# Kernel tuning notes

Hardware: AMD Instinct MI355X
Metric: run time of the kernel (lower is better)

## Reference

```python
import jax, jax.numpy as jnp
import numpy as np

NUM_EXPERTS = 8
TOP_K = 2
D_IN = 1024
D_OUT = 1024
N_TOKENS = 8192


def setup_inputs() -> dict:
    key = jax.random.key(0)
    ks = jax.random.split(key, 7)
    s_in = 1.0 / np.sqrt(D_IN)
    s_out = 1.0 / np.sqrt(D_OUT)
    return {
        "x": jax.random.normal(ks[0], (N_TOKENS, D_IN), dtype=jnp.float32),
        # stacked expert params: fc1 [E, D_in, D_out], fc2 [E, D_out, D_out]
        "W1": jax.random.uniform(ks[1], (NUM_EXPERTS, D_IN, D_OUT), jnp.float32, -s_in, s_in),
        "b1": jax.random.uniform(ks[2], (NUM_EXPERTS, D_OUT), jnp.float32, -s_in, s_in),
        "W2": jax.random.uniform(ks[3], (NUM_EXPERTS, D_OUT, D_OUT), jnp.float32, -s_out, s_out),
        "b2": jax.random.uniform(ks[4], (NUM_EXPERTS, D_OUT), jnp.float32, -s_out, s_out),
        "Wg": jax.random.uniform(ks[5], (D_IN, NUM_EXPERTS), jnp.float32, -s_in, s_in),
        "bg": jax.random.uniform(ks[6], (NUM_EXPERTS,), jnp.float32, -s_in, s_in),
    }


def reference(x, W1, b1, W2, b2, Wg, bg):
    n = x.shape[0]
    # gating
    gate_logits = x @ Wg + bg                      # [N, E]
    gate_weights = jax.nn.softmax(gate_logits, axis=1)
    if TOP_K < NUM_EXPERTS:
        topk_vals, topk_idx = jax.lax.top_k(gate_weights, TOP_K)  # [N, K]
        rows = jnp.arange(n)[:, None]
        gate_weights = jnp.zeros_like(gate_weights).at[rows, topk_idx].set(topk_vals)
    # dense all-expert MLP fan-out (faithful to the original wasteful compute)
    h = jax.nn.relu(jnp.einsum('nd,edh->enh', x, W1) + b1[:, None, :])  # [E, N, H]
    y = jnp.einsum('enh,eho->eno', h, W2) + b2[:, None, :]               # [E, N, O]
    # weighted combine over experts
    out = jnp.einsum('ne,eno->no', gate_weights, y)                      # [N, O]
    return out
```

## Files before the change

kernel.cpp:

```cpp
#include <hip/hip_runtime.h>

#define NUM_E 8
#define N_TOK 8192
#define DIM 1024

typedef __attribute__((ext_vector_type(8))) short short8;
typedef __attribute__((ext_vector_type(4))) float f32x4;

__device__ __forceinline__ unsigned short f2bf(float f) {
  unsigned int u = __float_as_uint(f);
  u = (u + 0x7fffu + ((u >> 16) & 1u)) >> 16;
  return (unsigned short)u;
}

__device__ __forceinline__ void async16(const unsigned short* g, unsigned short* l) {
  __builtin_amdgcn_global_load_lds((const __attribute__((address_space(1))) void*)g,
                                   (__attribute__((address_space(3))) void*)l,
                                   16, 0, 0);
}

__global__ __launch_bounds__(256) void convert_w_kernel(const float* __restrict__ W1,
                                                        const float* __restrict__ W2,
                                                        unsigned short* __restrict__ W1T,
                                                        unsigned short* __restrict__ W2T) {
  int tid = blockIdx.x * 256 + threadIdx.x;
  int n   = tid & 1023;
  int kc  = (tid >> 10) & 127;
  int mat = tid >> 17;
  const float* src;
  unsigned short* dst;
  if (mat < 8) { src = W1 + (size_t)mat * (DIM * DIM); dst = W1T + (size_t)mat * (DIM * DIM); }
  else         { src = W2 + (size_t)(mat - 8) * (DIM * DIM); dst = W2T + (size_t)(mat - 8) * (DIM * DIM); }
  const int k0 = kc * 8;
  union { unsigned short u[8]; uint4 v; } o;
#pragma unroll
  for (int j = 0; j < 8; ++j)
    o.u[j] = f2bf(src[(size_t)(k0 + j) * DIM + n]);
  *(uint4*)(dst + (size_t)n * DIM + k0) = o.v;
}

__global__ __launch_bounds__(256) void gate1_kernel(const float* __restrict__ x,
                                                    const float* __restrict__ Wg,
                                                    const float* __restrict__ bg,
                                                    int* __restrict__ tok_top,
                                                    float2* __restrict__ tok_wts,
                                                    unsigned short* __restrict__ xb) {
  const int wave = threadIdx.x >> 6;
  const int lane = threadIdx.x & 63;
  const int n = blockIdx.x * 4 + wave;
  const float4* xr = (const float4*)(x + (size_t)n * DIM);
  unsigned short* xbr = xb + (size_t)n * DIM;
  float acc[NUM_E];
#pragma unroll
  for (int e = 0; e < NUM_E; ++e) acc[e] = 0.f;
#pragma unroll
  for (int it = 0; it < 4; ++it) {
    float4 xv = xr[it * 64 + lane];
    const float4* wr = (const float4*)Wg + (size_t)(it * 256 + lane * 4) * 2;
    float xs[4] = {xv.x, xv.y, xv.z, xv.w};
    union { unsigned short u[4]; uint2 v; } oo;
    oo.u[0] = f2bf(xv.x); oo.u[1] = f2bf(xv.y);
    oo.u[2] = f2bf(xv.z); oo.u[3] = f2bf(xv.w);
    *(uint2*)(xbr + it * 256 + lane * 4) = oo.v;
#pragma unroll
    for (int dd = 0; dd < 4; ++dd) {
      float4 wa = wr[dd * 2 + 0];
      float4 wb = wr[dd * 2 + 1];
      acc[0] += xs[dd] * wa.x; acc[1] += xs[dd] * wa.y;
      acc[2] += xs[dd] * wa.z; acc[3] += xs[dd] * wa.w;
      acc[4] += xs[dd] * wb.x; acc[5] += xs[dd] * wb.y;
      acc[6] += xs[dd] * wb.z; acc[7] += xs[dd] * wb.w;
    }
  }
#pragma unroll
  for (int e = 0; e < NUM_E; ++e)
#pragma unroll
    for (int off = 32; off > 0; off >>= 1)
      acc[e] += __shfl_down(acc[e], off);
  if (lane == 0) {
    float p[NUM_E];
    float mx = -1e30f;
#pragma unroll
    for (int e = 0; e < NUM_E; ++e) { p[e] = acc[e] + bg[e]; mx = fmaxf(mx, p[e]); }
    float s = 0.f;
#pragma unroll
    for (int e = 0; e < NUM_E; ++e) { p[e] = expf(p[e] - mx); s += p[e]; }
    float inv = 1.f / s;
    int i0 = 0;
#pragma unroll
    for (int e = 1; e < NUM_E; ++e) if (p[e] > p[i0]) i0 = e;
    int i1 = (i0 == 0) ? 1 : 0;
#pragma unroll
    for (int e = 0; e < NUM_E; ++e) if (e != i0 && p[e] > p[i1]) i1 = e;
    tok_top[n] = i0 | (i1 << 8);
    tok_wts[n] = make_float2(p[i0] * inv, p[i1] * inv);
  }
}

__global__ __launch_bounds__(1024) void gate2_kernel(const int* __restrict__ tok_top,
                                                     const float2* __restrict__ tok_wts,
                                                     int* __restrict__ counts,
                                                     int* __restrict__ tok_idx,
                                                     float* __restrict__ tok_w) {
  const int e = blockIdx.x;
  const int t = threadIdx.x;
  const int lane = t & 63;
  const int wave = t >> 6;
  __shared__ int wsum[16];
  __shared__ int blocktot;
  int match[8];
  float w[8];
  int cnt = 0;
#pragma unroll
  for (int j = 0; j < 8; ++j) {
    int n = t * 8 + j;
    int top = tok_top[n];
    float2 ww = tok_wts[n];
    bool m0 = (top & 0xff) == e;
    bool m1 = ((top >> 8) & 0xff) == e;
    match[j] = (m0 || m1) ? 1 : 0;
    w[j] = m0 ? ww.x : ww.y;
    cnt += match[j];
  }
  int inc = cnt;
#pragma unroll
  for (int off = 1; off < 64; off <<= 1) {
    int v = __shfl_up(inc, off);
    if (lane >= off) inc += v;
  }
  if (lane == 63) wsum[wave] = inc;
  __syncthreads();
  if (t < 16) {
    int v = wsum[t];
    int s = v;
#pragma unroll
    for (int off = 1; off < 16; off <<= 1) {
      int u = __shfl_up(s, off);
      if (lane >= off) s += u;
    }
    wsum[t] = s - v;
    if (t == 15) blocktot = s;
  }
  __syncthreads();
  int slot = wsum[wave] + inc - cnt;
#pragma unroll
  for (int j = 0; j < 8; ++j) {
    if (match[j]) {
      tok_idx[e * N_TOK + slot] = t * 8 + j;
      tok_w[e * N_TOK + slot] = w[j];
      slot++;
    }
  }
  if (t == 0) counts[e] = blocktot;
}


template <bool FC1>
__global__ __launch_bounds__(256, 3) void moe_gemm_kernel(
    const unsigned short* __restrict__ A_src,
    const unsigned short* __restrict__ wT,
    const float* __restrict__ bias,
    const int* __restrict__ counts,
    const int* __restrict__ tok_idx,
    const float* __restrict__ tok_w,
    unsigned short* __restrict__ h_out,
    float* __restrict__ out)
{
  const int e = blockIdx.x;
  const int count = counts[e];
  const int m0 = blockIdx.z * 128;
  if (m0 >= count) return;
  const int n0 = blockIdx.y * 128;

  int base = 0;
#pragma unroll
  for (int i = 0; i < NUM_E; ++i) base += (i < e) ? ((counts[i] + 127) & ~127) : 0;

  const int tid  = threadIdx.x;
  const int wave = tid >> 6;
  const int lane = tid & 63;
  const int l15  = lane & 15;
  const int quad = lane >> 4;
  const int wm   = wave & 1;
  const int wn   = wave >> 1;

  __shared__ unsigned short sA[3][128 * 32];
  __shared__ unsigned short sB[3][128 * 32];
  __shared__ int   s_tok[128];
  __shared__ float s_w[128];

  if (!FC1) {
    if (tid < 128) {
      int slot = m0 + tid;
      int cs = slot < count ? slot : count - 1;
      s_tok[tid] = tok_idx[e * N_TOK + cs];
      s_w[tid]   = slot < count ? tok_w[e * N_TOK + slot] : 0.f;
    }
    __syncthreads();
  }

  const int r0 = 32 * wave + l15;
  const int r1 = r0 + 16;
  size_t aOff0, aOff1;
  if (FC1) {
    int s0 = m0 + r0; s0 = s0 < count ? s0 : count - 1;
    int s1 = m0 + r1; s1 = s1 < count ? s1 : count - 1;
    aOff0 = (size_t)tok_idx[e * N_TOK + s0] * DIM;
    aOff1 = (size_t)tok_idx[e * N_TOK + s1] * DIM;
  } else {
    aOff0 = (size_t)(base + m0 + r0) * DIM;
    aOff1 = (size_t)(base + m0 + r1) * DIM;
  }
  const unsigned short* wte = wT + (size_t)e * DIM * DIM;
  const size_t bOff0 = (size_t)(n0 + r0) * DIM;
  const size_t bOff1 = (size_t)(n0 + r1) * DIM;
  const int kl = quad * 8;
  const int c0 = (2 * wave + 0) * 512;
  const int c1 = (2 * wave + 1) * 512;

  const f32x4 vzero = {0.f, 0.f, 0.f, 0.f};
  f32x4 acc[4][4];
#pragma unroll
  for (int i = 0; i < 4; ++i)
#pragma unroll
    for (int j = 0; j < 4; ++j) acc[i][j] = vzero;

  auto stage = [&](int kt, int b) {
    const int koff = kt * 32 + kl;
    async16(A_src + aOff0 + koff, &sA[b][c0]);
    async16(A_src + aOff1 + koff, &sA[b][c1]);
    async16(wte + bOff0 + koff, &sB[b][c0]);
    async16(wte + bOff1 + koff, &sB[b][c1]);
  };

  stage(0, 0);
  stage(1, 1);
#pragma unroll
  for (int kt = 0; kt < 32; ++kt) {
    const int cur = kt % 3;
    if (kt + 1 < 32) {
      asm volatile("s_waitcnt vmcnt(4)\n\ts_barrier" ::: "memory");
    } else {
      asm volatile("s_waitcnt vmcnt(0)\n\ts_barrier" ::: "memory");
    }
    if (kt + 2 < 32) stage(kt + 2, (kt + 2) % 3);
    short8 af[4], bfr[4];
#pragma unroll
    for (int i = 0; i < 4; ++i)
      af[i] = *(const short8*)&sA[cur][(wm * 4 + i) * 512 + lane * 8];
#pragma unroll
    for (int j = 0; j < 4; ++j)
      bfr[j] = *(const short8*)&sB[cur][(wn * 4 + j) * 512 + lane * 8];
#pragma unroll
    for (int i = 0; i < 4; ++i)
#pragma unroll
      for (int j = 0; j < 4; ++j)
        acc[i][j] = __builtin_amdgcn_mfma_f32_16x16x32_bf16(af[i], bfr[j], acc[i][j], 0, 0, 0);
  }

  float bv[4];
#pragma unroll
  for (int j = 0; j < 4; ++j)
    bv[j] = bias[e * DIM + n0 + (wn * 4 + j) * 16 + l15];

  if (FC1) {
#pragma unroll
    for (int i = 0; i < 4; ++i) {
      const int rbase = (wm * 4 + i) * 16 + quad * 4;
#pragma unroll
      for (int r = 0; r < 4; ++r) {
        const int slot = m0 + rbase + r;
        if (slot < count) {
          unsigned short* hp = h_out + (size_t)(base + slot) * DIM + n0;
#pragma unroll
          for (int j = 0; j < 4; ++j) {
            float v = acc[i][j][r] + bv[j];
            v = v > 0.f ? v : 0.f;
            hp[(wn * 4 + j) * 16 + l15] = f2bf(v);
          }
        }
      }
    }
  } else {
#pragma unroll
    for (int i = 0; i < 4; ++i) {
      const int rbase = (wm * 4 + i) * 16 + quad * 4;
#pragma unroll
      for (int r = 0; r < 4; ++r) {
        const int slot = m0 + rbase + r;
        if (slot < count) {
          const int rl = rbase + r;
          const int tok = s_tok[rl];
          const float w = s_w[rl];
          float* op = out + (size_t)tok * DIM + n0;
#pragma unroll
          for (int j = 0; j < 4; ++j) {
            float v = acc[i][j][r] + bv[j];
            atomicAdd(&op[(wn * 4 + j) * 16 + l15], w * v);
          }
        }
      }
    }
  }
}


extern "C" void kernel_launch(void* const* d_in, const int* in_sizes, int n_in,
                              void* d_out, int out_size, void* d_ws, size_t ws_size,
                              hipStream_t stream) {
  const float* x  = (const float*)d_in[0];
  const float* W1 = (const float*)d_in[1];
  const float* b1 = (const float*)d_in[2];
  const float* W2 = (const float*)d_in[3];
  const float* b2 = (const float*)d_in[4];
  const float* Wg = (const float*)d_in[5];
  const float* bg = (const float*)d_in[6];
  float* out = (float*)d_out;

  char* ws = (char*)d_ws;
  int*            counts  = (int*)(ws);
  int*            tok_idx = (int*)(ws + 1024);
  float*          tok_w   = (float*)(ws + 263168);
  unsigned short* xb      = (unsigned short*)(ws + 525312);
  unsigned short* w1t     = (unsigned short*)(ws + 525312 + 16777216ull);
  unsigned short* w2t     = (unsigned short*)(ws + 525312 + 2ull * 16777216ull);
  unsigned short* hb      = (unsigned short*)(ws + 525312 + 3ull * 16777216ull);
  size_t gate_off = 525312 + 3ull * 16777216ull + 35651584ull;
  int*            tok_top = (int*)(ws + gate_off);
  float2*         tok_wts = (float2*)(ws + gate_off + 32768);

  hipMemsetAsync(d_out, 0, (size_t)N_TOK * DIM * sizeof(float), stream);

  convert_w_kernel<<<2 * NUM_E * DIM * (DIM / 8) / 256, 256, 0, stream>>>(W1, W2, w1t, w2t);
  gate1_kernel<<<N_TOK / 4, 256, 0, stream>>>(x, Wg, bg, tok_top, tok_wts, xb);
  gate2_kernel<<<NUM_E, 1024, 0, stream>>>(tok_top, tok_wts, counts, tok_idx, tok_w);
  moe_gemm_kernel<true><<<dim3(NUM_E, 8, 64), 256, 0, stream>>>(
      xb, w1t, b1, counts, tok_idx, tok_w, hb, nullptr);
  moe_gemm_kernel<false><<<dim3(NUM_E, 8, 64), 256, 0, stream>>>(
      hb, w2t, b2, counts, tok_idx, tok_w, nullptr, out);
}
```

Baseline: 398.8 us.

## Fuse weight convert and gating into one prep kernel; compact MoE tile grid

```diff
diff --git a/kernel.cpp b/kernel.cpp
--- a/kernel.cpp
+++ b/kernel.cpp
@@ -19,81 +19,91 @@
                                    16, 0, 0);
 }
 
-__global__ __launch_bounds__(256) void convert_w_kernel(const float* __restrict__ W1,
-                                                        const float* __restrict__ W2,
-                                                        unsigned short* __restrict__ W1T,
-                                                        unsigned short* __restrict__ W2T) {
-  int tid = blockIdx.x * 256 + threadIdx.x;
-  int n   = tid & 1023;
-  int kc  = (tid >> 10) & 127;
-  int mat = tid >> 17;
-  const float* src;
-  unsigned short* dst;
-  if (mat < 8) { src = W1 + (size_t)mat * (DIM * DIM); dst = W1T + (size_t)mat * (DIM * DIM); }
-  else         { src = W2 + (size_t)(mat - 8) * (DIM * DIM); dst = W2T + (size_t)(mat - 8) * (DIM * DIM); }
-  const int k0 = kc * 8;
-  union { unsigned short u[8]; uint4 v; } o;
-#pragma unroll
-  for (int j = 0; j < 8; ++j)
-    o.u[j] = f2bf(src[(size_t)(k0 + j) * DIM + n]);
-  *(uint4*)(dst + (size_t)n * DIM + k0) = o.v;
-}
-
-__global__ __launch_bounds__(256) void gate1_kernel(const float* __restrict__ x,
-                                                    const float* __restrict__ Wg,
-                                                    const float* __restrict__ bg,
-                                                    int* __restrict__ tok_top,
-                                                    float2* __restrict__ tok_wts,
-                                                    unsigned short* __restrict__ xb) {
-  const int wave = threadIdx.x >> 6;
-  const int lane = threadIdx.x & 63;
-  const int n = blockIdx.x * 4 + wave;
-  const float4* xr = (const float4*)(x + (size_t)n * DIM);
-  unsigned short* xbr = xb + (size_t)n * DIM;
-  float acc[NUM_E];
-#pragma unroll
-  for (int e = 0; e < NUM_E; ++e) acc[e] = 0.f;
-#pragma unroll
-  for (int it = 0; it < 4; ++it) {
-    float4 xv = xr[it * 64 + lane];
-    const float4* wr = (const float4*)Wg + (size_t)(it * 256 + lane * 4) * 2;
-    float xs[4] = {xv.x, xv.y, xv.z, xv.w};
-    union { unsigned short u[4]; uint2 v; } oo;
-    oo.u[0] = f2bf(xv.x); oo.u[1] = f2bf(xv.y);
-    oo.u[2] = f2bf(xv.z); oo.u[3] = f2bf(xv.w);
-    *(uint2*)(xbr + it * 256 + lane * 4) = oo.v;
-#pragma unroll
-    for (int dd = 0; dd < 4; ++dd) {
-      float4 wa = wr[dd * 2 + 0];
-      float4 wb = wr[dd * 2 + 1];
-      acc[0] += xs[dd] * wa.x; acc[1] += xs[dd] * wa.y;
-      acc[2] += xs[dd] * wa.z; acc[3] += xs[dd] * wa.w;
-      acc[4] += xs[dd] * wb.x; acc[5] += xs[dd] * wb.y;
-      acc[6] += xs[dd] * wb.z; acc[7] += xs[dd] * wb.w;
-    }
-  }
-#pragma unroll
-  for (int e = 0; e < NUM_E; ++e)
-#pragma unroll
-    for (int off = 32; off > 0; off >>= 1)
-      acc[e] += __shfl_down(acc[e], off);
-  if (lane == 0) {
-    float p[NUM_E];
-    float mx = -1e30f;
-#pragma unroll
-    for (int e = 0; e < NUM_E; ++e) { p[e] = acc[e] + bg[e]; mx = fmaxf(mx, p[e]); }
-    float s = 0.f;
-#pragma unroll
-    for (int e = 0; e < NUM_E; ++e) { p[e] = expf(p[e] - mx); s += p[e]; }
-    float inv = 1.f / s;
-    int i0 = 0;
-#pragma unroll
-    for (int e = 1; e < NUM_E; ++e) if (p[e] > p[i0]) i0 = e;
-    int i1 = (i0 == 0) ? 1 : 0;
-#pragma unroll
-    for (int e = 0; e < NUM_E; ++e) if (e != i0 && p[e] > p[i1]) i1 = e;
-    tok_top[n] = i0 | (i1 << 8);
-    tok_wts[n] = make_float2(p[i0] * inv, p[i1] * inv);
+__global__ __launch_bounds__(256) void prep_kernel(
+    const float* __restrict__ W1, const float* __restrict__ W2,
+    unsigned short* __restrict__ W1T, unsigned short* __restrict__ W2T,
+    const float* __restrict__ x, const float* __restrict__ Wg,
+    const float* __restrict__ bg, int* __restrict__ tok_top,
+    float2* __restrict__ tok_wts, unsigned short* __restrict__ xb) {
+  __shared__ float s[64][65];
+  if (blockIdx.x < 4096) {
+    const int bx  = blockIdx.x;
+    const int mat = bx >> 8;
+    const int tk  = (bx >> 4) & 15;
+    const int tn  = bx & 15;
+    const float* src;
+    unsigned short* dst;
+    if (mat < 8) { src = W1 + (size_t)mat * (DIM * DIM); dst = W1T + (size_t)mat * (DIM * DIM); }
+    else         { src = W2 + (size_t)(mat - 8) * (DIM * DIM); dst = W2T + (size_t)(mat - 8) * (DIM * DIM); }
+    const int k0 = tk * 64, n0 = tn * 64;
+    const int t = threadIdx.x;
+    const int nr = t & 63, wr = t >> 6;
+#pragma unroll
+    for (int i = 0; i < 16; ++i) {
+      int k = i * 4 + wr;
+      s[nr][k] = src[(size_t)(k0 + k) * DIM + n0 + nr];
+    }
+    __syncthreads();
+    const int kq = (t & 15) * 4, nw = t >> 4;
+#pragma unroll
+    for (int i = 0; i < 4; ++i) {
+      int n = i * 16 + nw;
+      ushort4 o;
+      o.x = f2bf(s[n][kq + 0]); o.y = f2bf(s[n][kq + 1]);
+      o.z = f2bf(s[n][kq + 2]); o.w = f2bf(s[n][kq + 3]);
+      *(ushort4*)(dst + (size_t)(n0 + n) * DIM + k0 + kq) = o;
+    }
+  } else {
+    const int wave = threadIdx.x >> 6;
+    const int lane = threadIdx.x & 63;
+    const int n = (blockIdx.x - 4096) * 4 + wave;
+    const float4* xr = (const float4*)(x + (size_t)n * DIM);
+    unsigned short* xbr = xb + (size_t)n * DIM;
+    float acc[NUM_E];
+#pragma unroll
+    for (int e = 0; e < NUM_E; ++e) acc[e] = 0.f;
+#pragma unroll
+    for (int it = 0; it < 4; ++it) {
+      float4 xv = xr[it * 64 + lane];
+      const float4* wr = (const float4*)Wg + (size_t)(it * 256 + lane * 4) * 2;
+      float xs[4] = {xv.x, xv.y, xv.z, xv.w};
+      union { unsigned short u[4]; uint2 v; } oo;
+      oo.u[0] = f2bf(xv.x); oo.u[1] = f2bf(xv.y);
+      oo.u[2] = f2bf(xv.z); oo.u[3] = f2bf(xv.w);
+      *(uint2*)(xbr + it * 256 + lane * 4) = oo.v;
+#pragma unroll
+      for (int dd = 0; dd < 4; ++dd) {
+        float4 wa = wr[dd * 2 + 0];
+        float4 wb = wr[dd * 2 + 1];
+        acc[0] += xs[dd] * wa.x; acc[1] += xs[dd] * wa.y;
+        acc[2] += xs[dd] * wa.z; acc[3] += xs[dd] * wa.w;
+        acc[4] += xs[dd] * wb.x; acc[5] += xs[dd] * wb.y;
+        acc[6] += xs[dd] * wb.z; acc[7] += xs[dd] * wb.w;
+      }
+    }
+#pragma unroll
+    for (int e = 0; e < NUM_E; ++e)
+#pragma unroll
+      for (int off = 32; off > 0; off >>= 1)
+        acc[e] += __shfl_down(acc[e], off);
+    if (lane == 0) {
+      float p[NUM_E];
+      float mx = -1e30f;
+#pragma unroll
+      for (int e = 0; e < NUM_E; ++e) { p[e] = acc[e] + bg[e]; mx = fmaxf(mx, p[e]); }
+      float ss = 0.f;
+#pragma unroll
+      for (int e = 0; e < NUM_E; ++e) { p[e] = expf(p[e] - mx); ss += p[e]; }
+      float inv = 1.f / ss;
+      int i0 = 0;
+#pragma unroll
+      for (int e = 1; e < NUM_E; ++e) if (p[e] > p[i0]) i0 = e;
+      int i1 = (i0 == 0) ? 1 : 0;
+#pragma unroll
+      for (int e = 0; e < NUM_E; ++e) if (e != i0 && p[e] > p[i1]) i1 = e;
+      tok_top[n] = i0 | (i1 << 8);
+      tok_wts[n] = make_float2(p[i0] * inv, p[i1] * inv);
+    }
   }
 }
 
@@ -166,15 +176,24 @@
     unsigned short* __restrict__ h_out,
     float* __restrict__ out)
 {
-  const int e = blockIdx.x;
+  const int y = blockIdx.y;
+  int e = -1, m0 = 0, base = 0;
+  {
+    int acc_tiles = 0, acc_rows = 0;
+#pragma unroll
+    for (int i = 0; i < NUM_E; ++i) {
+      int c = counts[i];
+      int t = (c + 127) >> 7;
+      if (y >= acc_tiles && y < acc_tiles + t) {
+        e = i; m0 = (y - acc_tiles) * 128; base = acc_rows;
+      }
+      acc_tiles += t;
+      acc_rows += t * 128;
+    }
+  }
+  if (e < 0) return;
   const int count = counts[e];
-  const int m0 = blockIdx.z * 128;
-  if (m0 >= count) return;
-  const int n0 = blockIdx.y * 128;
-
-  int base = 0;
-#pragma unroll
-  for (int i = 0; i < NUM_E; ++i) base += (i < e) ? ((counts[i] + 127) & ~127) : 0;
+  const int n0 = blockIdx.x * 128;
 
   const int tid  = threadIdx.x;
   const int wave = tid >> 6;
@@ -184,19 +203,16 @@
   const int wm   = wave & 1;
   const int wn   = wave >> 1;
 
-  __shared__ unsigned short sA[3][128 * 32];
-  __shared__ unsigned short sB[3][128 * 32];
+  __shared__ unsigned short sA[2 * 4096];
+  __shared__ unsigned short sB[2 * 4096];
   __shared__ int   s_tok[128];
   __shared__ float s_w[128];
 
-  if (!FC1) {
-    if (tid < 128) {
-      int slot = m0 + tid;
-      int cs = slot < count ? slot : count - 1;
-      s_tok[tid] = tok_idx[e * N_TOK + cs];
-      s_w[tid]   = slot < count ? tok_w[e * N_TOK + slot] : 0.f;
-    }
-    __syncthreads();
+  if (!FC1 && tid < 128) {
+    int slot = m0 + tid;
+    int cs = slot < count ? slot : count - 1;
+    s_tok[tid] = tok_idx[e * N_TOK + cs];
+    s_w[tid]   = slot < count ? tok_w[e * N_TOK + slot] : 0.f;
   }
 
   const int r0 = 32 * wave + l15;
@@ -225,37 +241,32 @@
 #pragma unroll
     for (int j = 0; j < 4; ++j) acc[i][j] = vzero;
 
-  auto stage = [&](int kt, int b) {
-    const int koff = kt * 32 + kl;
-    async16(A_src + aOff0 + koff, &sA[b][c0]);
-    async16(A_src + aOff1 + koff, &sA[b][c1]);
-    async16(wte + bOff0 + koff, &sB[b][c0]);
-    async16(wte + bOff1 + koff, &sB[b][c1]);
-  };
-
-  stage(0, 0);
-  stage(1, 1);
-#pragma unroll
-  for (int kt = 0; kt < 32; ++kt) {
-    const int cur = kt % 3;
-    if (kt + 1 < 32) {
-      asm volatile("s_waitcnt vmcnt(4)\n\ts_barrier" ::: "memory");
-    } else {
-      asm volatile("s_waitcnt vmcnt(0)\n\ts_barrier" ::: "memory");
-    }
-    if (kt + 2 < 32) stage(kt + 2, (kt + 2) % 3);
-    short8 af[4], bfr[4];
-#pragma unroll
-    for (int i = 0; i < 4; ++i)
-      af[i] = *(const short8*)&sA[cur][(wm * 4 + i) * 512 + lane * 8];
-#pragma unroll
-    for (int j = 0; j < 4; ++j)
-      bfr[j] = *(const short8*)&sB[cur][(wn * 4 + j) * 512 + lane * 8];
-#pragma unroll
-    for (int i = 0; i < 4; ++i)
+  for (int k0 = 0; k0 < DIM; k0 += 64) {
+    async16(A_src + aOff0 + k0 + kl,      &sA[c0]);
+    async16(A_src + aOff1 + k0 + kl,      &sA[c1]);
+    async16(A_src + aOff0 + k0 + 32 + kl, &sA[4096 + c0]);
+    async16(A_src + aOff1 + k0 + 32 + kl, &sA[4096 + c1]);
+    async16(wte + bOff0 + k0 + kl,        &sB[c0]);
+    async16(wte + bOff1 + k0 + kl,        &sB[c1]);
+    async16(wte + bOff0 + k0 + 32 + kl,   &sB[4096 + c0]);
+    async16(wte + bOff1 + k0 + 32 + kl,   &sB[4096 + c1]);
+    __syncthreads();
+#pragma unroll
+    for (int s = 0; s < 2; ++s) {
+      short8 af[4], bfr[4];
+#pragma unroll
+      for (int i = 0; i < 4; ++i)
+        af[i] = *(const short8*)&sA[s * 4096 + (wm * 4 + i) * 512 + lane * 8];
 #pragma unroll
       for (int j = 0; j < 4; ++j)
-        acc[i][j] = __builtin_amdgcn_mfma_f32_16x16x32_bf16(af[i], bfr[j], acc[i][j], 0, 0, 0);
+        bfr[j] = *(const short8*)&sB[s * 4096 + (wn * 4 + j) * 512 + lane * 8];
+#pragma unroll
+      for (int i = 0; i < 4; ++i)
+#pragma unroll
+        for (int j = 0; j < 4; ++j)
+          acc[i][j] = __builtin_amdgcn_mfma_f32_16x16x32_bf16(af[i], bfr[j], acc[i][j], 0, 0, 0);
+    }
+    __syncthreads();
   }
 
   float bv[4];
@@ -331,11 +342,11 @@
 
   hipMemsetAsync(d_out, 0, (size_t)N_TOK * DIM * sizeof(float), stream);
 
-  convert_w_kernel<<<2 * NUM_E * DIM * (DIM / 8) / 256, 256, 0, stream>>>(W1, W2, w1t, w2t);
-  gate1_kernel<<<N_TOK / 4, 256, 0, stream>>>(x, Wg, bg, tok_top, tok_wts, xb);
+  prep_kernel<<<4096 + 2048, 256, 0, stream>>>(W1, W2, w1t, w2t,
+                                               x, Wg, bg, tok_top, tok_wts, xb);
   gate2_kernel<<<NUM_E, 1024, 0, stream>>>(tok_top, tok_wts, counts, tok_idx, tok_w);
-  moe_gemm_kernel<true><<<dim3(NUM_E, 8, 64), 256, 0, stream>>>(
+  moe_gemm_kernel<true><<<dim3(8, 136), 256, 0, stream>>>(
       xb, w1t, b1, counts, tok_idx, tok_w, hb, nullptr);
-  moe_gemm_kernel<false><<<dim3(NUM_E, 8, 64), 256, 0, stream>>>(
+  moe_gemm_kernel<false><<<dim3(8, 136), 256, 0, stream>>>(
       hb, w2t, b2, counts, tok_idx, tok_w, nullptr, out);
 }
```

Result: faster. 373.0 us (-6.5%).
